# Kernel optimization log

Hardware: AMD Instinct MI355X
Metric: run time of the kernel (lower is better)

Reference implementation:

```python
import jax, jax.numpy as jnp
import numpy as np

EPS = 1e-6

def setup_inputs() -> dict:
    key = jax.random.key(0)
    k1, k2 = jax.random.split(key)
    b, seq, d = 4, 512, 64
    x = jax.random.normal(k1, (b, seq, d, d), dtype=jnp.float32)
    # diagonal decay rates in (0, 1): realistic SSM decay, positive like the clamped param
    A = jax.random.uniform(k2, (d,), dtype=jnp.float32)
    return {"x": x, "A": A}

def reference(x, A):
    b, seq, d, _ = x.shape
    log_A = jnp.log(jnp.clip(A, EPS))                      # (d,)
    # cumsum over seq of the (constant-in-time) log decay, as in the original
    cs_A = jnp.cumsum(jnp.broadcast_to(log_A, (seq, d)), axis=0)  # (seq, d)
    log_M = cs_A[:, None, :] - cs_A[None, :, :]            # (t, j, d)
    idx = jnp.arange(seq)
    mask = idx[:, None] >= idx[None, :]                    # causal: t >= j
    M = jnp.where(mask[:, :, None], jnp.exp(log_M), 0.0)   # (t, j, d)
    # A is batch-independent, so M is shared across batch (same math as the original)
    out = jnp.einsum('tjr,bjrc->btrc', M, x)               # (b, seq, d, d)
    return out
```

## Files before the change

kernel.cpp:

```cpp
#include <hip/hip_runtime.h>


#define B_    4
#define SEQ_  512
#define D_    64
#define CH_   8
#define NCH_  (SEQ_ / CH_)
#define NCQ_  (D_ / 4)
#define NTHR_ (NCH_ * NCQ_)

__global__ __launch_bounds__(NTHR_) void ssm_scan_kernel(
    const float* __restrict__ x, const float* __restrict__ A,
    float* __restrict__ out)
{
    __shared__ float4 Elds[NCH_][NCQ_];

    const int blk = blockIdx.x;
    const int bi  = blk >> 6;
    const int r   = blk & 63;
    const int tid = threadIdx.x;
    const int ch  = tid >> 4;
    const int cq  = tid & 15;

    const float a = fmaxf(A[r], 1e-6f);

    const int j0 = ch * CH_;
    const size_t base = ((size_t)(bi * SEQ_ + j0) * D_ + r) * D_ + cq * 4;
    const float4* xp = (const float4*)(x + base);
    float4*       op = (float4*)(out + base);
    const int jstride4 = (D_ * D_) / 4;

    float4 loc[CH_];
    float s0 = 0.f, s1 = 0.f, s2 = 0.f, s3 = 0.f;
    #pragma unroll
    for (int t = 0; t < CH_; ++t) {
        float4 v = xp[(size_t)t * jstride4];
        s0 = fmaf(s0, a, v.x);
        s1 = fmaf(s1, a, v.y);
        s2 = fmaf(s2, a, v.z);
        s3 = fmaf(s3, a, v.w);
        loc[t] = make_float4(s0, s1, s2, s3);
    }

    Elds[ch][cq] = make_float4(s0, s1, s2, s3);
    __syncthreads();

    float a2 = a * a, a4 = a2 * a2, aL = a4 * a4;

    float c0 = 0.f, c1 = 0.f, c2 = 0.f, c3 = 0.f;
    for (int cp = 0; cp < ch; ++cp) {
        float4 e = Elds[cp][cq];
        c0 = fmaf(c0, aL, e.x);
        c1 = fmaf(c1, aL, e.y);
        c2 = fmaf(c2, aL, e.z);
        c3 = fmaf(c3, aL, e.w);
    }

    float p = a;
    #pragma unroll
    for (int t = 0; t < CH_; ++t) {
        float4 l = loc[t];
        float4 o;
        o.x = fmaf(c0, p, l.x);
        o.y = fmaf(c1, p, l.y);
        o.z = fmaf(c2, p, l.z);
        o.w = fmaf(c3, p, l.w);
        op[(size_t)t * jstride4] = o;
        p *= a;
    }
}

extern "C" void kernel_launch(void* const* d_in, const int* in_sizes, int n_in,
                              void* d_out, int out_size, void* d_ws, size_t ws_size,
                              hipStream_t stream) {
    const float* x   = (const float*)d_in[0];
    const float* A   = (const float*)d_in[1];
    float*       out = (float*)d_out;

    dim3 grid(B_ * D_);
    dim3 block(NTHR_);
    hipLaunchKernelGGL(ssm_scan_kernel, grid, block, 0, stream, x, A, out);
}
```

Measured before the change: 82.58 us.

## Split sequence chunks across blocks with cooperative grid sync for carry propagation

```diff
diff --git a/kernel.cpp b/kernel.cpp
--- a/kernel.cpp
+++ b/kernel.cpp
@@ -1,40 +1,39 @@
 #include <hip/hip_runtime.h>
+#include <hip/hip_cooperative_groups.h>
+
+namespace cg = cooperative_groups;
 
 
-#define B_    4
-#define SEQ_  512
-#define D_    64
-#define CH_   8
-#define NCH_  (SEQ_ / CH_)
-#define NCQ_  (D_ / 4)
-#define NTHR_ (NCH_ * NCQ_)
+#define B_     4
+#define SEQ_   512
+#define D_     64
+#define PLANE_ (D_ * D_)
+#define PQ_    (PLANE_ / 4)
+#define CH_    8
+#define NCH_   (SEQ_ / CH_)
+#define NTHR_  1024
+#define GRID_  (B_ * NCH_)
 
-__global__ __launch_bounds__(NTHR_) void ssm_scan_kernel(
+__global__ __launch_bounds__(NTHR_, 4) void ssm_coop_ws(
     const float* __restrict__ x, const float* __restrict__ A,
-    float* __restrict__ out)
+    float* __restrict__ out, float* __restrict__ E)
 {
-    __shared__ float4 Elds[NCH_][NCQ_];
-
     const int blk = blockIdx.x;
     const int bi  = blk >> 6;
-    const int r   = blk & 63;
-    const int tid = threadIdx.x;
-    const int ch  = tid >> 4;
-    const int cq  = tid & 15;
+    const int m   = blk & (NCH_ - 1);
+    const int k   = threadIdx.x;
+    const int r   = k >> 4;
 
     const float a = fmaxf(A[r], 1e-6f);
 
-    const int j0 = ch * CH_;
-    const size_t base = ((size_t)(bi * SEQ_ + j0) * D_ + r) * D_ + cq * 4;
-    const float4* xp = (const float4*)(x + base);
-    float4*       op = (float4*)(out + base);
-    const int jstride4 = (D_ * D_) / 4;
+    const float4* xp = (const float4*)x + (size_t)(bi * SEQ_ + m * CH_) * PQ_ + k;
+    float4*       op = (float4*)out     + (size_t)(bi * SEQ_ + m * CH_) * PQ_ + k;
 
     float4 loc[CH_];
     float s0 = 0.f, s1 = 0.f, s2 = 0.f, s3 = 0.f;
-    #pragma unroll
+#pragma unroll
     for (int t = 0; t < CH_; ++t) {
-        float4 v = xp[(size_t)t * jstride4];
+        float4 v = xp[t * PQ_];
         s0 = fmaf(s0, a, v.x);
         s1 = fmaf(s1, a, v.y);
         s2 = fmaf(s2, a, v.z);
@@ -42,14 +41,15 @@
         loc[t] = make_float4(s0, s1, s2, s3);
     }
 
-    Elds[ch][cq] = make_float4(s0, s1, s2, s3);
-    __syncthreads();
+    ((float4*)E)[(size_t)(bi * NCH_ + m) * PQ_ + k] = make_float4(s0, s1, s2, s3);
+
+    cg::this_grid().sync();
 
     float a2 = a * a, a4 = a2 * a2, aL = a4 * a4;
-
     float c0 = 0.f, c1 = 0.f, c2 = 0.f, c3 = 0.f;
-    for (int cp = 0; cp < ch; ++cp) {
-        float4 e = Elds[cp][cq];
+    const float4* Eb = (const float4*)E + (size_t)bi * NCH_ * PQ_ + k;
+    for (int mp = 0; mp < m; ++mp) {
+        float4 e = Eb[(size_t)mp * PQ_];
         c0 = fmaf(c0, aL, e.x);
         c1 = fmaf(c1, aL, e.y);
         c2 = fmaf(c2, aL, e.z);
@@ -57,15 +57,65 @@
     }
 
     float p = a;
-    #pragma unroll
+#pragma unroll
     for (int t = 0; t < CH_; ++t) {
         float4 l = loc[t];
-        float4 o;
-        o.x = fmaf(c0, p, l.x);
-        o.y = fmaf(c1, p, l.y);
-        o.z = fmaf(c2, p, l.z);
-        o.w = fmaf(c3, p, l.w);
-        op[(size_t)t * jstride4] = o;
+        op[t * PQ_] = make_float4(fmaf(c0, p, l.x), fmaf(c1, p, l.y),
+                                  fmaf(c2, p, l.z), fmaf(c3, p, l.w));
+        p *= a;
+    }
+}
+
+__global__ __launch_bounds__(NTHR_, 4) void ssm_coop_planes(
+    const float* __restrict__ x, const float* __restrict__ A,
+    float* __restrict__ out)
+{
+    const int blk = blockIdx.x;
+    const int bi  = blk >> 6;
+    const int m   = blk & (NCH_ - 1);
+    const int k   = threadIdx.x;
+    const int r   = k >> 4;
+
+    const float a = fmaxf(A[r], 1e-6f);
+
+    const float4* xp = (const float4*)x + (size_t)(bi * SEQ_ + m * CH_) * PQ_ + k;
+    float4*       op = (float4*)out     + (size_t)(bi * SEQ_ + m * CH_) * PQ_ + k;
+
+    float4 loc[CH_];
+    float s0 = 0.f, s1 = 0.f, s2 = 0.f, s3 = 0.f;
+#pragma unroll
+    for (int t = 0; t < CH_; ++t) {
+        float4 v = xp[t * PQ_];
+        s0 = fmaf(s0, a, v.x);
+        s1 = fmaf(s1, a, v.y);
+        s2 = fmaf(s2, a, v.z);
+        s3 = fmaf(s3, a, v.w);
+        loc[t] = make_float4(s0, s1, s2, s3);
+    }
+
+    op[(CH_ - 1) * PQ_] = make_float4(s0, s1, s2, s3);
+
+    cg::this_grid().sync();
+
+    float a2 = a * a, a4 = a2 * a2, aL = a4 * a4;
+    float c0 = 0.f, c1 = 0.f, c2 = 0.f, c3 = 0.f;
+    const float4* Eb = (const float4*)out + ((size_t)bi * SEQ_ + (CH_ - 1)) * PQ_ + k;
+    for (int mp = 0; mp < m; ++mp) {
+        float4 e = Eb[(size_t)mp * CH_ * PQ_];
+        c0 = fmaf(c0, aL, e.x);
+        c1 = fmaf(c1, aL, e.y);
+        c2 = fmaf(c2, aL, e.z);
+        c3 = fmaf(c3, aL, e.w);
+    }
+
+    cg::this_grid().sync();
+
+    float p = a;
+#pragma unroll
+    for (int t = 0; t < CH_; ++t) {
+        float4 l = loc[t];
+        op[t * PQ_] = make_float4(fmaf(c0, p, l.x), fmaf(c1, p, l.y),
+                                  fmaf(c2, p, l.z), fmaf(c3, p, l.w));
         p *= a;
     }
 }
@@ -77,7 +127,16 @@
     const float* A   = (const float*)d_in[1];
     float*       out = (float*)d_out;
 
-    dim3 grid(B_ * D_);
-    dim3 block(NTHR_);
-    hipLaunchKernelGGL(ssm_scan_kernel, grid, block, 0, stream, x, A, out);
+    const size_t eBytes = sizeof(float) * (size_t)B_ * NCH_ * PLANE_;
+
+    if (d_ws != nullptr && ws_size >= eBytes) {
+        float* E = (float*)d_ws;
+        void* args[] = {(void*)&x, (void*)&A, (void*)&out, (void*)&E};
+        hipLaunchCooperativeKernel((void*)ssm_coop_ws, dim3(GRID_), dim3(NTHR_),
+                                   args, 0, stream);
+    } else {
+        void* args[] = {(void*)&x, (void*)&A, (void*)&out};
+        hipLaunchCooperativeKernel((void*)ssm_coop_planes, dim3(GRID_), dim3(NTHR_),
+                                   args, 0, stream);
+    }
 }
```

Measured after the change: 299.8 us. 3.63x slower.
